# Performance work log

Measured on AMD Instinct MI355X. Metric: run time of the kernel, lower is better.

## Reference

```python
import jax, jax.numpy as jnp
import numpy as np

B, S, D = 1, 2048, 3072
H, DH = 24, 128
ENC, NIP = 512, 64
COND = (512 // 8) * (512 // 8) * 16 // 64  # 1024 cond tokens per lora
RANK, ALPHA, LW, IP_SCALE = 16, 16.0, 1.0, 1.0
EPS = 1e-5


def _rms(x):
    return x * jax.lax.rsqrt(jnp.mean(x * x, axis=-1, keepdims=True) + EPS)


def _to_heads(x):
    b, s, _ = x.shape
    return x.reshape(b, s, H, DH).transpose(0, 2, 1, 3)  # [B,H,S,DH]


def _from_heads(x):
    b, h, s, d = x.shape
    return x.transpose(0, 2, 1, 3).reshape(b, s, h * d)


def _lora(x, dn, up):
    # token mask keeps only the cond block (number=0, n_loras=1 -> last COND tokens)
    y = ((x[:, -COND:, :] @ dn) @ up) * (ALPHA / RANK)
    z = jnp.zeros((x.shape[0], x.shape[1] - COND, up.shape[1]), x.dtype)
    return jnp.concatenate([z, y], axis=1)


def _sdpa(q, k, v, mask=None):
    s = jnp.einsum('bhqd,bhkd->bhqk', q, k) * (1.0 / np.sqrt(DH))
    if mask is not None:
        s = s + mask
    return jnp.einsum('bhqk,bhkd->bhqd', jax.nn.softmax(s, axis=-1), v)


def _forward(hidden_states, encoder_hidden_states, image_emb,
             Wq, bq, Wk, bk, Wv, bv, Waq, baq, Wak, bak, Wav, bav,
             Wo, bo, Wao, bao, Wkip, Wvip,
             lq_dn, lq_up, lk_dn, lk_up, lv_dn, lv_up, lp_dn, lp_up):
    hs, ehs, img = hidden_states, encoder_hidden_states, image_emb
    # context (encoder) projections + RMSNorm on q/k
    eq = _rms(_to_heads(ehs @ Waq + baq))
    ek = _rms(_to_heads(ehs @ Wak + bak))
    ev = _to_heads(ehs @ Wav + bav)
    # main-stream q/k/v with masked LoRA branches
    q = hs @ Wq + bq + LW * _lora(hs, lq_dn, lq_up)
    k = hs @ Wk + bk + LW * _lora(hs, lk_dn, lk_up)
    v = hs @ Wv + bv + LW * _lora(hs, lv_dn, lv_up)
    q = _rms(_to_heads(q))
    k = _rms(_to_heads(k))
    v = _to_heads(v)
    # IP-adapter branch: extra K/V from image_emb, norm_added_k is RMSNorm(128)
    kip = _rms(_to_heads(img @ Wkip))
    vip = _to_heads(img @ Wvip)
    ip_out = _from_heads(_sdpa(q, kip, vip))  # [B,S,D]
    # concat encoder stream ahead of main stream
    q = jnp.concatenate([eq, q], axis=2)
    k = jnp.concatenate([ek, k], axis=2)
    v = jnp.concatenate([ev, v], axis=2)
    SL = ENC + S
    SB = SL - COND  # scaled_block_size
    m = jnp.ones((SL, SL), jnp.float32)
    m = m.at[:SB, :].set(0.0)        # non-cond rows attend everywhere
    m = m.at[SB:, SB:].set(0.0)      # single cond block attends to itself (n_loras=1)
    mask = m * (-1e20)
    out = _from_heads(_sdpa(q, k, v, mask))  # [B,SL,D]
    enc_out = out[:, :ENC, :]
    main = out[:, ENC:, :] + IP_SCALE * ip_out
    main = main @ Wo + bo
    main = main + LW * _lora(main, lp_dn, lp_up)  # proj LoRA (to_out dropout=identity)
    enc_out = enc_out @ Wao + bao
    return jnp.concatenate([enc_out, main], axis=1)  # [B, ENC+S, D]


def setup_inputs():
    key = jax.random.key(0)
    ks = iter(jax.random.split(key, 40))
    w = lambda *sh: jax.random.normal(next(ks), sh, jnp.float32) * 0.02
    return dict(
        hidden_states=jax.random.normal(next(ks), (B, S, D), jnp.float32),
        encoder_hidden_states=jax.random.normal(next(ks), (B, ENC, D), jnp.float32),
        image_emb=jax.random.normal(next(ks), (B, NIP, D), jnp.float32),
        Wq=w(D, D), bq=w(D), Wk=w(D, D), bk=w(D), Wv=w(D, D), bv=w(D),
        Waq=w(D, D), baq=w(D), Wak=w(D, D), bak=w(D), Wav=w(D, D), bav=w(D),
        Wo=w(D, D), bo=w(D), Wao=w(D, D), bao=w(D),
        Wkip=w(D, D), Wvip=w(D, D),
        lq_dn=w(D, RANK), lq_up=w(RANK, D), lk_dn=w(D, RANK), lk_up=w(RANK, D),
        lv_dn=w(D, RANK), lv_up=w(RANK, D), lp_dn=w(D, RANK), lp_up=w(RANK, D),
    )


def reference(hidden_states, encoder_hidden_states, image_emb,
              Wq, bq, Wk, bk, Wv, bv, Waq, baq, Wak, bak, Wav, bav,
              Wo, bo, Wao, bao, Wkip, Wvip,
              lq_dn, lq_up, lk_dn, lk_up, lv_dn, lv_up, lp_dn, lp_up):
    return _forward(hidden_states, encoder_hidden_states, image_emb,
                    Wq, bq, Wk, bk, Wv, bv, Waq, baq, Wak, bak, Wav, bav,
                    Wo, bo, Wao, bao, Wkip, Wvip,
                    lq_dn, lq_up, lk_dn, lk_up, lv_dn, lv_up, lp_dn, lp_up)
```

## Files before the change

### kernel.cpp

```cpp
#include <hip/hip_runtime.h>

typedef unsigned short u16;
typedef short s16x8 __attribute__((ext_vector_type(8)));
typedef float f32x4 __attribute__((ext_vector_type(4)));
typedef const __attribute__((address_space(1))) unsigned int* as1_u32p;
typedef __attribute__((address_space(3))) unsigned int* as3_u32p;

static_assert(sizeof(s16x8) == 16, "");

struct alignas(8) U16x4 { u16 x, y, z, w; };

__device__ __forceinline__ u16 f2bf(float f) {
  union { float f; unsigned u; } c; c.f = f;
  return (u16)((c.u + 0x7fffu + ((c.u >> 16) & 1u)) >> 16);
}
__device__ __forceinline__ float bf2f(u16 h) {
  union { unsigned u; float f; } c; c.u = ((unsigned)h) << 16;
  return c.f;
}
__device__ __forceinline__ void async16(const void* g, void* l) {
  __builtin_amdgcn_global_load_lds((as1_u32p)g, (as3_u32p)l, 16, 0, 0);
}

__launch_bounds__(256)
__global__ void lora_dn3(const float* __restrict__ X, int ldx,
                         const float* __restrict__ d0, const float* __restrict__ d1,
                         const float* __restrict__ d2, float* __restrict__ t) {
  __shared__ float red[4][48];
  const int m = blockIdx.x;
  const float* xr = X + (long)m * ldx;
  float p[48];
#pragma unroll
  for (int r = 0; r < 48; ++r) p[r] = 0.f;
  for (int k = threadIdx.x; k < 3072; k += 256) {
    float a = xr[k];
    const float* e0 = d0 + (long)k * 16;
    const float* e1 = d1 + (long)k * 16;
    const float* e2 = d2 + (long)k * 16;
#pragma unroll
    for (int r = 0; r < 16; ++r) {
      p[r]      += a * e0[r];
      p[16 + r] += a * e1[r];
      p[32 + r] += a * e2[r];
    }
  }
#pragma unroll
  for (int r = 0; r < 48; ++r)
#pragma unroll
    for (int st = 1; st < 64; st <<= 1) p[r] += __shfl_xor(p[r], st, 64);
  int lane = threadIdx.x & 63, w = threadIdx.x >> 6;
  if (lane == 0) {
#pragma unroll
    for (int r = 0; r < 48; ++r) red[w][r] = p[r];
  }
  __syncthreads();
  if (threadIdx.x < 48) {
    int r = threadIdx.x;
    t[(long)m * 48 + r] = red[0][r] + red[1][r] + red[2][r] + red[3][r];
  }
}

__launch_bounds__(256)
__global__ void mega_prep(const float* __restrict__ Waq, const float* __restrict__ Wak,
                          const float* __restrict__ Wav, const float* __restrict__ Wq,
                          const float* __restrict__ Wk, const float* __restrict__ Wv,
                          u16* __restrict__ WTbE, u16* __restrict__ WTbM,
                          const float* __restrict__ Wo, const float* __restrict__ bo,
                          const float* __restrict__ lp_dn, float* __restrict__ Wod,
                          const float* __restrict__ hs, const float* __restrict__ tl,
                          u16* __restrict__ hsb,
                          const float* __restrict__ ehs, u16* __restrict__ ehsb,
                          const float* __restrict__ img, u16* __restrict__ imgb,
                          const float* __restrict__ baq, const float* __restrict__ bak,
                          const float* __restrict__ bav, const float* __restrict__ bq,
                          const float* __restrict__ bk, const float* __restrict__ bv,
                          float* __restrict__ bpk,
                          const float* __restrict__ u0, const float* __restrict__ u1,
                          const float* __restrict__ u2) {
  __shared__ char lmem[4352];
  const int b = blockIdx.x;
  if (b < 55296) {
    int mat = b / 9216, tile = b % 9216;
    const float* src = (mat == 0) ? Waq : (mat == 1) ? Wak : (mat == 2) ? Wav
                       : (mat == 3) ? Wq : (mat == 4) ? Wk : Wv;
    u16* dst = (mat < 3) ? WTbE + (long)mat * 3072 * 3072
                         : WTbM + (long)(mat - 3) * 3072 * 3136;
    const int ldd = (mat < 3) ? 3072 : 3136;
    float (*tile2)[33] = (float(*)[33])lmem;
    int k0 = (tile / 96) * 32, n0 = (tile % 96) * 32;
    int r = threadIdx.x >> 3, c4 = (threadIdx.x & 7) * 4;
    float4 v = *(const float4*)(src + (long)(k0 + r) * 3072 + n0 + c4);
    tile2[r][c4 + 0] = v.x; tile2[r][c4 + 1] = v.y;
    tile2[r][c4 + 2] = v.z; tile2[r][c4 + 3] = v.w;
    __syncthreads();
    U16x4 o{f2bf(tile2[c4 + 0][r]), f2bf(tile2[c4 + 1][r]),
            f2bf(tile2[c4 + 2][r]), f2bf(tile2[c4 + 3][r])};
    *(U16x4*)(dst + (long)(n0 + r) * ldd + k0 + c4) = o;
  } else if (b < 58369) {
    const int m = b - 55296;
    float (*red)[16] = (float(*)[16])lmem;
    const float* xr = (m < 3072) ? Wo + (long)m * 3072 : bo;
    float p[16];
#pragma unroll
    for (int r = 0; r < 16; ++r) p[r] = 0.f;
    for (int k = threadIdx.x; k < 3072; k += 256) {
      float a = xr[k];
      const float* d = lp_dn + (long)k * 16;
#pragma unroll
      for (int r = 0; r < 16; ++r) p[r] += a * d[r];
    }
#pragma unroll
    for (int r = 0; r < 16; ++r)
#pragma unroll
      for (int st = 1; st < 64; st <<= 1) p[r] += __shfl_xor(p[r], st, 64);
    int lane = threadIdx.x & 63, w = threadIdx.x >> 6;
    if (lane == 0) {
#pragma unroll
      for (int r = 0; r < 16; ++r) red[w][r] = p[r];
    }
    __syncthreads();
    if (threadIdx.x < 16) {
      int r = threadIdx.x;
      Wod[(long)m * 16 + r] = red[0][r] + red[1][r] + red[2][r] + red[3][r];
    }
  } else {
    const int pb = b - 58369;
    if (pb < 3136) {
      long idx = (long)pb * 256 + threadIdx.x;
      long m = idx / 392, c = idx % 392;
      U16x4 o0, o1;
      if (c < 384) {
        const float* p = hs + m * 3072 + c * 8;
        float4 a = *(const float4*)p;
        float4 bb = *(const float4*)(p + 4);
        o0 = U16x4{f2bf(a.x), f2bf(a.y), f2bf(a.z), f2bf(a.w)};
        o1 = U16x4{f2bf(bb.x), f2bf(bb.y), f2bf(bb.z), f2bf(bb.w)};
      } else {
        u16 t[8];
#pragma unroll
        for (int i = 0; i < 8; ++i) {
          int r = (int)(c - 384) * 8 + i;
          float v = (m >= 1024 && r < 48) ? tl[(m - 1024) * 48 + r] : 0.f;
          t[i] = f2bf(v);
        }
        o0 = U16x4{t[0], t[1], t[2], t[3]};
        o1 = U16x4{t[4], t[5], t[6], t[7]};
      }
      u16* d = hsb + m * 3136 + c * 8;
      *(U16x4*)d = o0;
      *(U16x4*)(d + 4) = o1;
    } else if (pb < 3904) {
      long i = ((long)(pb - 3136) * 256 + threadIdx.x) * 8;
      float4 a = *(const float4*)(ehs + i);
      float4 bb = *(const float4*)(ehs + i + 4);
      *(U16x4*)(ehsb + i) = U16x4{f2bf(a.x), f2bf(a.y), f2bf(a.z), f2bf(a.w)};
      *(U16x4*)(ehsb + i + 4) = U16x4{f2bf(bb.x), f2bf(bb.y), f2bf(bb.z), f2bf(bb.w)};
    } else if (pb < 4000) {
      long i = ((long)(pb - 3904) * 256 + threadIdx.x) * 8;
      float4 a = *(const float4*)(img + i);
      float4 bb = *(const float4*)(img + i + 4);
      *(U16x4*)(imgb + i) = U16x4{f2bf(a.x), f2bf(a.y), f2bf(a.z), f2bf(a.w)};
      *(U16x4*)(imgb + i + 4) = U16x4{f2bf(bb.x), f2bf(bb.y), f2bf(bb.z), f2bf(bb.w)};
    } else if (pb < 4072) {
      int i = (pb - 4000) * 256 + threadIdx.x;
      if (i < 9216)
        bpk[i] = (i < 3072) ? baq[i] : (i < 6144) ? bak[i - 3072] : bav[i - 6144];
      else {
        int j = i - 9216;
        bpk[i] = (j < 3072) ? bq[j] : (j < 6144) ? bk[j - 3072] : bv[j - 6144];
      }
    } else {
      int idx = (pb - 4072) * 256 + threadIdx.x;
      int n = idx >> 6, i = idx & 63;
      int seg = n / 3072;
      const float* up = (seg == 0) ? u0 : (seg == 1) ? u1 : u2;
      int r = i - seg * 16;
      float v = (r >= 0 && r < 16) ? up[(long)r * 3072 + (n - seg * 3072)] : 0.f;
      WTbM[(long)n * 3136 + 3072 + i] = f2bf(v);
    }
  }
}

struct WT2 { const float* src[2]; u16* dst[2]; };

__launch_bounds__(256)
__global__ void transpose_kv(WT2 args) {
  const float* src = args.src[blockIdx.z];
  u16* dst = args.dst[blockIdx.z];
  __shared__ float tile[32][33];
  int k0 = blockIdx.x * 32, n0 = blockIdx.y * 32;
  int r = threadIdx.x >> 3, c4 = (threadIdx.x & 7) * 4;
  float4 v = *(const float4*)(src + (long)(k0 + r) * 3072 + n0 + c4);
  tile[r][c4 + 0] = v.x; tile[r][c4 + 1] = v.y;
  tile[r][c4 + 2] = v.z; tile[r][c4 + 3] = v.w;
  __syncthreads();
  U16x4 o{f2bf(tile[c4 + 0][r]), f2bf(tile[c4 + 1][r]),
          f2bf(tile[c4 + 2][r]), f2bf(tile[c4 + 3][r])};
  *(U16x4*)(dst + (long)(n0 + r) * 3072 + k0 + c4) = o;
}

__launch_bounds__(256)
__global__ void t_tail(u16* __restrict__ At, const float* __restrict__ Wod) {
  __shared__ float red[4][16];
  const int tok = blockIdx.x;
  u16* tail = At + (long)(512 + tok) * 3136 + 3072;
  if (tok < 1024) {
    if (threadIdx.x < 64) tail[threadIdx.x] = 0;
    return;
  }
  const u16* xr = At + (long)(512 + tok) * 3136;
  float p[16];
#pragma unroll
  for (int r = 0; r < 16; ++r) p[r] = 0.f;
  for (int n = threadIdx.x; n < 3072; n += 256) {
    float a = bf2f(xr[n]);
    const float* wd = Wod + (long)n * 16;
#pragma unroll
    for (int r = 0; r < 16; ++r) p[r] += a * wd[r];
  }
#pragma unroll
  for (int r = 0; r < 16; ++r)
#pragma unroll
    for (int st = 1; st < 64; st <<= 1) p[r] += __shfl_xor(p[r], st, 64);
  int lane = threadIdx.x & 63, w = threadIdx.x >> 6;
  if (lane == 0) {
#pragma unroll
    for (int r = 0; r < 16; ++r) red[w][r] = p[r];
  }
  __syncthreads();
  if (threadIdx.x < 64) {
    if (threadIdx.x < 16) {
      int r = threadIdx.x;
      float t = red[0][r] + red[1][r] + red[2][r] + red[3][r] + Wod[3072L * 16 + r];
      tail[r] = f2bf(t);
    } else {
      tail[threadIdx.x] = 0;
    }
  }
}

template <int BM, int MI, int NI>
__launch_bounds__(256)
__global__ void gemm_f32(const u16* __restrict__ A, int lda,
                         const u16* __restrict__ B, int ldb,
                         float* __restrict__ C, int ldc,
                         const float* __restrict__ bias, int KC, long cstride) {
  constexpr int WCOLS = 128 / (NI * 16);
  constexpr int ABYTES = BM * 128;
  __shared__ char smem[ABYTES + 128 * 128];
  char* As = smem;
  char* Bs = smem + ABYTES;
  const int tid = threadIdx.x;
  const int w = tid >> 6, lane = tid & 63;
  const int lr = lane & 15, lg = lane >> 4;
  const int wr = w / WCOLS, wc = w % WCOLS;
  const int nbx = gridDim.x;
  const int nwg = nbx * gridDim.y;
  const int flat = blockIdx.y * nbx + blockIdx.x;
  const int swz = (flat & 7) * (nwg >> 3) + (flat >> 3);
  const long m0 = (long)(swz % nbx) * BM;
  const long n0 = (long)(swz / nbx) * 128;
  const int k0 = blockIdx.z * KC;
  C += blockIdx.z * cstride;
  f32x4 acc[MI][NI] = {};
  constexpr int ACH = BM / 32;
  for (int kb = k0; kb < k0 + KC; kb += 64) {
    __syncthreads();
#pragma unroll
    for (int i = 0; i < ACH; ++i) {
      int x = (tid + 256 * i) * 16;
      int row = x >> 7;
// ... 202 lines not shown
          int tok = wr * 64 + mi * 16 + lg * 4 + j;
          *(u16*)(smem + tok * 256 + (d2 ^ ((tok & 7) << 4))) =
              f2bf(acc[mi][ni][j] * scl[mi][j]);
        }
      }
  } else {
#pragma unroll
    for (int mi = 0; mi < 4; ++mi)
#pragma unroll
      for (int ni = 0; ni < 4; ++ni) {
        int d = wc * 64 + ni * 16 + lr;
        int tok0b = (wr * 64 + mi * 16 + lg * 4) * 2;
        U16x4 o{f2bf(acc[mi][ni][0]), f2bf(acc[mi][ni][1]),
                f2bf(acc[mi][ni][2]), f2bf(acc[mi][ni][3])};
        *(U16x4*)(smem + d * 256 + (tok0b ^ ((d & 7) << 4))) = o;
      }
  }
  __syncthreads();
#pragma unroll
  for (int i = 0; i < 8; ++i) {
    int x = (tid + 256 * i) * 16;
    int row = x >> 8, col = x & 255;
    s16x8 vdat = *(const s16x8*)(smem + row * 256 + (col ^ ((row & 7) << 4)));
    if (seg < 2) {
      u16* g = (seg == 0 ? Qo : Ko) + ((long)head * 2560 + t0 + m0 + row) * 128;
      *(s16x8*)((char*)g + col) = vdat;
    } else {
      u16* g = VTo + ((long)head * 128 + row) * 2560 + t0 + m0;
      *(s16x8*)((char*)g + col) = vdat;
    }
  }
}

__launch_bounds__(256)
__global__ void gemm_out(const u16* __restrict__ Atok, const u16* __restrict__ Benc,
                         const u16* __restrict__ Bmain, float* __restrict__ outp,
                         const float* __restrict__ bao, const float* __restrict__ bo) {
  __shared__ char smem[128 * 128 + 128 * 128];
  char* As = smem;
  char* Bs = smem + 128 * 128;
  const int tid = threadIdx.x;
  const int w = tid >> 6, lane = tid & 63;
  const int lr = lane & 15, lg = lane >> 4;
  const int wr = w >> 1, wc = w & 1;
  const int flat = blockIdx.y * 20 + blockIdx.x;
  const int swz = (flat & 7) * 60 + (flat >> 3);
  const int mx = swz % 20;
  const long n0 = (long)(swz / 20) * 128;
  const u16* A;
  const u16* B;
  const float* bias;
  float* C;
  int ldb, K;
  long m0;
  if (mx < 4) {
    A = Atok; B = Benc; ldb = 3072; K = 3072; bias = bao; C = outp;
    m0 = (long)mx * 128;
  } else {
    A = Atok + 512L * 3136; B = Bmain; ldb = 3136; K = 3136; bias = bo;
    C = outp + 512L * 3072; m0 = (long)(mx - 4) * 128;
  }
  f32x4 acc[4][4] = {};
  for (int kb = 0; kb < K; kb += 64) {
    __syncthreads();
#pragma unroll
    for (int i = 0; i < 4; ++i) {
// ... 15 lines not shown
#pragma unroll
    for (int kc = 0; kc < 2; ++kc) {
      s16x8 af[4], bfr[4];
#pragma unroll
      for (int mi = 0; mi < 4; ++mi) {
        int row = wr * 64 + mi * 16 + lr;
        int b = ((row << 7) + kc * 64 + lg * 16) ^ ((row & 7) << 4);
        af[mi] = *(const s16x8*)(As + b);
      }
#pragma unroll
      for (int ni = 0; ni < 4; ++ni) {
        int row = wc * 64 + ni * 16 + lr;
        int b = ((row << 7) + kc * 64 + lg * 16) ^ ((row & 7) << 4);
        bfr[ni] = *(const s16x8*)(Bs + b);
      }
#pragma unroll
      for (int mi = 0; mi < 4; ++mi)
#pragma unroll
        for (int ni = 0; ni < 4; ++ni)
          acc[mi][ni] = __builtin_amdgcn_mfma_f32_16x16x32_bf16(af[mi], bfr[ni], acc[mi][ni], 0, 0, 0);
    }
  }
#pragma unroll
  for (int mi = 0; mi < 4; ++mi) {
#pragma unroll
    for (int ni = 0; ni < 4; ++ni) {
      long col = n0 + wc * 64 + ni * 16 + lr;
      float bv = bias[col];
#pragma unroll
      for (int j = 0; j < 4; ++j) {
        long row = m0 + wr * 64 + mi * 16 + lg * 4 + j;
        C[row * 3072 + col] = acc[mi][ni][j] + bv;
      }
    }
  }
}

__launch_bounds__(512, 2)
__global__ void attn_mega(const u16* __restrict__ QB, const u16* __restrict__ KB,
                          const u16* __restrict__ VT, const u16* __restrict__ KipB,
                          const u16* __restrict__ VipT, u16* __restrict__ OutTok,
                          const float* __restrict__ Wao, const float* __restrict__ Wo,
                          u16* __restrict__ WTbE, u16* __restrict__ WTbM,
                          const float* __restrict__ lp_up) {
  __shared__ char smem[81920];
  const int bf = blockIdx.x;
  const int tid = threadIdx.x;
  if (bf >= 480) {
    if (bf < 9696) {
      int t2 = (bf - 480) * 2 + (tid >> 8);
      int mat = t2 / 9216, tile = t2 % 9216;
      const float* src = mat ? Wo : Wao;
      u16* dst = mat ? WTbM : WTbE;
      const int ldd = mat ? 3136 : 3072;
      float (*tl2)[32][33] = (float(*)[32][33])smem;
      int half = tid >> 8, lt = tid & 255;
      int k0 = (tile / 96) * 32, n0t = (tile % 96) * 32;
      int r = lt >> 3, c4 = (lt & 7) * 4;
      float4 v = *(const float4*)(src + (long)(k0 + r) * 3072 + n0t + c4);
      tl2[half][r][c4 + 0] = v.x; tl2[half][r][c4 + 1] = v.y;
      tl2[half][r][c4 + 2] = v.z; tl2[half][r][c4 + 3] = v.w;
      __syncthreads();
      U16x4 o{f2bf(tl2[half][c4 + 0][r]), f2bf(tl2[half][c4 + 1][r]),
              f2bf(tl2[half][c4 + 2][r]), f2bf(tl2[half][c4 + 3][r])};
      *(U16x4*)(dst + (long)(n0t + r) * ldd + k0 + c4) = o;
    } else {
      int idx = (bf - 9696) * 512 + tid;
      int n = idx >> 6, i = idx & 63;
      float v = (i < 16) ? lp_up[(long)i * 3072 + n] : 0.f;
      WTbM[(long)n * 3136 + 3072 + i] = f2bf(v);
    }
    return;
  }
  const int w = tid >> 6, lane = tid & 63;
  const int lr = lane & 15, lg = lane >> 4;
  int h, qb;
  if (bf < 288) { h = bf / 12; qb = bf % 12; }
  else { int s = bf - 288; h = s / 8; qb = 12 + s % 8; }
  const int q0 = qb * 128;
  const bool ip = (q0 >= 512);
  const u16* Qrow = QB + (long)(h * 2560 + q0 + w * 16 + lr) * 128;
  s16x8 qf[4];
#pragma unroll
  for (int dc = 0; dc < 4; ++dc) qf[dc] = *(const s16x8*)(Qrow + dc * 32 + lg * 8);
  f32x4 accO[8] = {};
  float l_r[4] = {0.f, 0.f, 0.f, 0.f};
  const int kv0 = (q0 >= 1536) ? 1536 : 0;
  const float sc = 0.08838834764831845f;

  auto stage_main = [&](int kv, int buf) {
#pragma unroll
    for (int i = 0; i < 2; ++i) {
      int x = (tid + 512 * i) * 16;
      int row = x >> 8;
      int sx = x ^ ((row & 7) << 4);
      async16((const char*)(KB + (long)(h * 2560 + kv + row) * 128) + (sx & 255),
              smem + buf * 16384 + ((i << 13) + (w << 10)));
    }
#pragma unroll
    for (int i = 0; i < 2; ++i) {
      int x = (tid + 512 * i) * 16;
      int row = x >> 7;
      int sx = x ^ ((row & 7) << 4);
      async16((const char*)(VT + (long)(h * 128 + row) * 2560 + kv) + (sx & 127),
              smem + 32768 + buf * 16384 + ((i << 13) + (w << 10)));
    }
  };
  auto stage_ip = [&](int buf) {
#pragma unroll
    for (int i = 0; i < 2; ++i) {
      int x = (tid + 512 * i) * 16;
      int row = x >> 8;
      int sx = x ^ ((row & 7) << 4);
      async16((const char*)(KipB + (long)(h * 64 + row) * 128) + (sx & 255),
              smem + buf * 16384 + ((i << 13) + (w << 10)));
    }
#pragma unroll
    for (int i = 0; i < 2; ++i) {
      int x = (tid + 512 * i) * 16;
      int row = x >> 7;
      int sx = x ^ ((row & 7) << 4);
      async16((const char*)(VipT + (long)(h * 128 + row) * 64) + (sx & 127),
              smem + 32768 + buf * 16384 + ((i << 13) + (w << 10)));
    }
  };

  stage_main(kv0, 0);
  __syncthreads();
  int cur = 0;
  for (int kv = kv0; kv < 2560; kv += 64) {
    if (kv + 64 < 2560) stage_main(kv + 64, cur ^ 1);
    else if (ip) stage_ip(cur ^ 1);
    const char* Ks = smem + cur * 16384;
    const char* Vs = smem + 32768 + cur * 16384;
    char* Pw = smem + 65536 + w * 2048;
    f32x4 s[4] = {};
    __builtin_amdgcn_s_setprio(1);
#pragma unroll
    for (int kt = 0; kt < 4; ++kt)
#pragma unroll
      for (int dc = 0; dc < 4; ++dc) {
        int row = kt * 16 + lr;
        int b = ((row << 8) + dc * 64 + lg * 16) ^ ((row & 7) << 4);
        s16x8 kf = *(const s16x8*)(Ks + b);
        s[kt] = __builtin_amdgcn_mfma_f32_16x16x32_bf16(qf[dc], kf, s[kt], 0, 0, 0);
      }
    __builtin_amdgcn_s_setprio(0);
#pragma unroll
    for (int kt = 0; kt < 4; ++kt)
#pragma unroll
      for (int j = 0; j < 4; ++j) {
        float pv = __expf(fmaf(s[kt][j], sc, -12.0f));
        l_r[j] += pv;
        int prow = lg * 4 + j;
        int b = ((prow << 7) + (kt * 16 + lr) * 2) ^ ((prow & 7) << 4);
        *(u16*)(Pw + b) = f2bf(pv);
      }
    asm volatile("s_waitcnt lgkmcnt(0)" ::: "memory");
    __builtin_amdgcn_s_setprio(1);
#pragma unroll
    for (int kc = 0; kc < 2; ++kc) {
      int pb = ((lr << 7) + kc * 64 + lg * 16) ^ ((lr & 7) << 4);
      s16x8 pf = *(const s16x8*)(Pw + pb);
#pragma unroll
      for (int dt = 0; dt < 8; ++dt) {
        int row = dt * 16 + lr;
        int b = ((row << 7) + kc * 64 + lg * 16) ^ ((row & 7) << 4);
        s16x8 vf = *(const s16x8*)(Vs + b);
        accO[dt] = __builtin_amdgcn_mfma_f32_16x16x32_bf16(pf, vf, accO[dt], 0, 0, 0);
      }
    }
    __builtin_amdgcn_s_setprio(0);
    __syncthreads();
    cur ^= 1;
  }
#pragma unroll
  for (int j = 0; j < 4; ++j) {
#pragma unroll
    for (int st = 1; st < 16; st <<= 1) l_r[j] += __shfl_xor(l_r[j], st, 16);
    l_r[j] = 1.f / l_r[j];
  }
#pragma unroll
  for (int dt = 0; dt < 8; ++dt)
#pragma unroll
    for (int j = 0; j < 4; ++j) accO[dt][j] *= l_r[j];
  if (ip) {
    const char* Ks = smem + cur * 16384;
    const char* Vs = smem + 32768 + cur * 16384;
    char* Pw = smem + 65536 + w * 2048;
    f32x4 s2[4] = {};
#pragma unroll
    for (int kt = 0; kt < 4; ++kt)
#pragma unroll
      for (int dc = 0; dc < 4; ++dc) {
        int row = kt * 16 + lr;
        int b = ((row << 8) + dc * 64 + lg * 16) ^ ((row & 7) << 4);
        s16x8 kf = *(const s16x8*)(Ks + b);
        s2[kt] = __builtin_amdgcn_mfma_f32_16x16x32_bf16(qf[dc], kf, s2[kt], 0, 0, 0);
      }
    float p2[4][4];
    float l2[4] = {0.f, 0.f, 0.f, 0.f};
#pragma unroll
    for (int kt = 0; kt < 4; ++kt)
#pragma unroll
      for (int j = 0; j < 4; ++j) {
        float pv = __expf(fmaf(s2[kt][j], sc, -12.0f));
        p2[kt][j] = pv;
        l2[j] += pv;
      }
#pragma unroll
    for (int j = 0; j < 4; ++j) {
#pragma unroll
      for (int st = 1; st < 16; st <<= 1) l2[j] += __shfl_xor(l2[j], st, 16);
      l2[j] = 1.f / l2[j];
    }
#pragma unroll
    for (int kt = 0; kt < 4; ++kt)
#pragma unroll
      for (int j = 0; j < 4; ++j) {
        int prow = lg * 4 + j;
        int b = ((prow << 7) + (kt * 16 + lr) * 2) ^ ((prow & 7) << 4);
        *(u16*)(Pw + b) = f2bf(p2[kt][j] * l2[j]);
      }
    asm volatile("s_waitcnt lgkmcnt(0)" ::: "memory");
#pragma unroll
    for (int kc = 0; kc < 2; ++kc) {
      int pb = ((lr << 7) + kc * 64 + lg * 16) ^ ((lr & 7) << 4);
      s16x8 pf = *(const s16x8*)(Pw + pb);
#pragma unroll
      for (int dt = 0; dt < 8; ++dt) {
        int row = dt * 16 + lr;
        int b = ((row << 7) + kc * 64 + lg * 16) ^ ((row & 7) << 4);
        s16x8 vf = *(const s16x8*)(Vs + b);
        accO[dt] = __builtin_amdgcn_mfma_f32_16x16x32_bf16(pf, vf, accO[dt], 0, 0, 0);
      }
    }
  }
#pragma unroll
  for (int j = 0; j < 4; ++j) {
    long tok = q0 + w * 16 + lg * 4 + j;
#pragma unroll
    for (int dt = 0; dt < 8; ++dt) {
      long col = h * 128 + dt * 16 + lr;
      OutTok[tok * 3136 + col] = f2bf(accO[dt][j]);
    }
  }
}


extern "C" void kernel_launch(void* const* d_in, const int* in_sizes, int n_in,
                              void* d_out, int out_size, void* d_ws, size_t ws_size,
                              hipStream_t stream) {
  const float* hs    = (const float*)d_in[0];
  const float* ehs   = (const float*)d_in[1];
  const float* img   = (const float*)d_in[2];
  const float* Wq    = (const float*)d_in[3];
  const float* bq    = (const float*)d_in[4];
  const float* Wk    = (const float*)d_in[5];
  const float* bk    = (const float*)d_in[6];
  const float* Wv    = (const float*)d_in[7];
  const float* bv    = (const float*)d_in[8];
  const float* Waq   = (const float*)d_in[9];
  const float* baq   = (const float*)d_in[10];
  const float* Wak   = (const float*)d_in[11];
  const float* bak   = (const float*)d_in[12];
  const float* Wav   = (const float*)d_in[13];
  const float* bav   = (const float*)d_in[14];
  const float* Wo    = (const float*)d_in[15];
  const float* bo    = (const float*)d_in[16];
  const float* Wao   = (const float*)d_in[17];
  const float* bao   = (const float*)d_in[18];
  const float* Wkip  = (const float*)d_in[19];
  const float* Wvip  = (const float*)d_in[20];
  const float* lq_dn = (const float*)d_in[21];
  const float* lq_up = (const float*)d_in[22];
  const float* lk_dn = (const float*)d_in[23];
  const float* lk_up = (const float*)d_in[24];
  const float* lv_dn = (const float*)d_in[25];
  const float* lv_up = (const float*)d_in[26];
  const float* lp_dn = (const float*)d_in[27];
  const float* lp_up = (const float*)d_in[28];
  float* outp = (float*)d_out;

  char* ws = (char*)d_ws;
  size_t off = 0;
  auto take = [&](size_t b) { char* p = ws + off; off += (b + 255) & ~(size_t)255; return p; };
  u16*   WTbE = (u16*)take(3LL * 3072 * 3072 * 2);
  u16*   WTbM = (u16*)take(3LL * 3072 * 3136 * 2);
  u16*   hsb  = (u16*)take(2048LL * 3136 * 2);
  u16*   ehsb = (u16*)take(512LL * 3072 * 2);
  u16*   imgb = (u16*)take(64LL * 3072 * 2);
  u16*   VTf  = (u16*)take(24LL * 128 * 2560 * 2);
  float* IP0  = (float*)take(4LL * 64 * 6144 * 4);
  u16*   KipB = (u16*)take(24LL * 64 * 128 * 2);
  u16*   VipB = (u16*)take(24LL * 64 * 128 * 2);
  u16*   VipT = (u16*)take(24LL * 128 * 64 * 2);
  float* bpk  = (float*)take(2 * 9216 * 4);
  float* tl   = (float*)take(1024LL * 48 * 4);
  float* Wod  = (float*)take(3073LL * 16 * 4);
  u16* QBf = (u16*)d_out;
  u16* KBf = (u16*)d_out + 24LL * 2560 * 128;
  u16* AttnTok = hsb;
  u16* E1 = WTbE + 3072LL * 3072;
  u16* E2 = WTbE + 2 * 3072LL * 3072;

  lora_dn3<<<1024, 256, 0, stream>>>(hs + 1024LL * 3072, 3072, lq_dn, lk_dn, lv_dn, tl);
  mega_prep<<<64745, 256, 0, stream>>>(Waq, Wak, Wav, Wq, Wk, Wv, WTbE, WTbM,
                                       Wo, bo, lp_dn, Wod,
                                       hs, tl, hsb, ehs, ehsb, img, imgb,
                                       baq, bak, bav, bq, bk, bv, bpk,
                                       lq_up, lk_up, lv_up);

  gemm_qkv<<<dim3(20, 72), 256, 0, stream>>>(ehsb, hsb, WTbE, WTbM, QBf, KBf, VTf, bpk);

  {
    WT2 a;
    a.src[0] = Wkip; a.dst[0] = E1;
    a.src[1] = Wvip; a.dst[1] = E2;
    transpose_kv<<<dim3(96, 96, 2), 256, 0, stream>>>(a);
  }
  gemm_f32<64, 4, 2><<<dim3(1, 48, 4), 256, 0, stream>>>(imgb, 3072, E1, 3072, IP0, 6144,
                                                          nullptr, 768, 64LL * 6144);
  rms_ip<<<128, 256, 0, stream>>>(IP0, KipB, VipB);
  transpose_v<<<dim3(2, 4, 24), 256, 0, stream>>>(VipB, VipT, 64);

  attn_mega<<<10080, 512, 0, stream>>>(QBf, KBf, VTf, KipB, VipT, AttnTok,
                                       Wao, Wo, WTbE, WTbM, lp_up);

  t_tail<<<2048, 256, 0, stream>>>(AttnTok, Wod);
  gemm_out<<<dim3(20, 24), 256, 0, stream>>>(AttnTok, WTbE, WTbM, outp, bao, bo);
}
```

Baseline: 577.2 us.

## Rebalance kernel fusion: fold LoRA-down into prep, split attention from weight transposes

Moves the LoRA down-projection into the mega_prep launch and adds a small t_hs kernel that writes its results into the hsb tail columns. The Wo/Wao transposes and lp_up packing move out of the attention mega-kernel into a new ttail_mega launch that also runs the tail projection, so attention now launches only its 480 compute blocks. Transpose_kv becomes a flat 1D grid. The aim is to stop the attention kernel from also carrying thousands of transpose blocks and to cut one launch, in exchange for an extra small kernel and different overlap between the transpose work and attention.

```diff
diff --git a/kernel.cpp b/kernel.cpp
--- a/kernel.cpp
+++ b/kernel.cpp
@@ -20,44 +20,6 @@
 }
 __device__ __forceinline__ void async16(const void* g, void* l) {
   __builtin_amdgcn_global_load_lds((as1_u32p)g, (as3_u32p)l, 16, 0, 0);
-}
-
-__launch_bounds__(256)
-__global__ void lora_dn3(const float* __restrict__ X, int ldx,
-                         const float* __restrict__ d0, const float* __restrict__ d1,
-                         const float* __restrict__ d2, float* __restrict__ t) {
-  __shared__ float red[4][48];
-  const int m = blockIdx.x;
-  const float* xr = X + (long)m * ldx;
-  float p[48];
-#pragma unroll
-  for (int r = 0; r < 48; ++r) p[r] = 0.f;
-  for (int k = threadIdx.x; k < 3072; k += 256) {
-    float a = xr[k];
-    const float* e0 = d0 + (long)k * 16;
-    const float* e1 = d1 + (long)k * 16;
-    const float* e2 = d2 + (long)k * 16;
-#pragma unroll
-    for (int r = 0; r < 16; ++r) {
-      p[r]      += a * e0[r];
-      p[16 + r] += a * e1[r];
-      p[32 + r] += a * e2[r];
-    }
-  }
-#pragma unroll
-  for (int r = 0; r < 48; ++r)
-#pragma unroll
-    for (int st = 1; st < 64; st <<= 1) p[r] += __shfl_xor(p[r], st, 64);
-  int lane = threadIdx.x & 63, w = threadIdx.x >> 6;
-  if (lane == 0) {
-#pragma unroll
-    for (int r = 0; r < 48; ++r) red[w][r] = p[r];
-  }
-  __syncthreads();
-  if (threadIdx.x < 48) {
-    int r = threadIdx.x;
-    t[(long)m * 48 + r] = red[0][r] + red[1][r] + red[2][r] + red[3][r];
-  }
 }
 
 __launch_bounds__(256)
@@ -67,8 +29,9 @@
                           u16* __restrict__ WTbE, u16* __restrict__ WTbM,
                           const float* __restrict__ Wo, const float* __restrict__ bo,
                           const float* __restrict__ lp_dn, float* __restrict__ Wod,
-                          const float* __restrict__ hs, const float* __restrict__ tl,
-                          u16* __restrict__ hsb,
+                          const float* __restrict__ d0, const float* __restrict__ d1,
+                          const float* __restrict__ d2, float* __restrict__ tl,
+                          const float* __restrict__ hs, u16* __restrict__ hsb,
                           const float* __restrict__ ehs, u16* __restrict__ ehsb,
                           const float* __restrict__ img, u16* __restrict__ imgb,
                           const float* __restrict__ baq, const float* __restrict__ bak,
@@ -96,8 +59,41 @@
     U16x4 o{f2bf(tile2[c4 + 0][r]), f2bf(tile2[c4 + 1][r]),
             f2bf(tile2[c4 + 2][r]), f2bf(tile2[c4 + 3][r])};
     *(U16x4*)(dst + (long)(n0 + r) * ldd + k0 + c4) = o;
-  } else if (b < 58369) {
+  } else if (b < 56320) {
     const int m = b - 55296;
+    float (*red)[48] = (float(*)[48])lmem;
+    const float* xr = hs + (long)(1024 + m) * 3072;
+    float p[48];
+#pragma unroll
+    for (int r = 0; r < 48; ++r) p[r] = 0.f;
+    for (int k = threadIdx.x; k < 3072; k += 256) {
+      float a = xr[k];
+      const float* e0 = d0 + (long)k * 16;
+      const float* e1 = d1 + (long)k * 16;
+      const float* e2 = d2 + (long)k * 16;
+#pragma unroll
+      for (int r = 0; r < 16; ++r) {
+        p[r]      += a * e0[r];
+        p[16 + r] += a * e1[r];
+        p[32 + r] += a * e2[r];
+      }
+    }
+#pragma unroll
+    for (int r = 0; r < 48; ++r)
+#pragma unroll
+      for (int st = 1; st < 64; st <<= 1) p[r] += __shfl_xor(p[r], st, 64);
+    int lane = threadIdx.x & 63, w = threadIdx.x >> 6;
+    if (lane == 0) {
+#pragma unroll
+      for (int r = 0; r < 48; ++r) red[w][r] = p[r];
+    }
+    __syncthreads();
+    if (threadIdx.x < 48) {
+      int r = threadIdx.x;
+      tl[(long)m * 48 + r] = red[0][r] + red[1][r] + red[2][r] + red[3][r];
+    }
+  } else if (b < 59393) {
+    const int m = b - 56320;
     float (*red)[16] = (float(*)[16])lmem;
     const float* xr = (m < 3072) ? Wo + (long)m * 3072 : bo;
     float p[16];
@@ -124,27 +120,17 @@
       Wod[(long)m * 16 + r] = red[0][r] + red[1][r] + red[2][r] + red[3][r];
     }
   } else {
-    const int pb = b - 58369;
+    const int pb = b - 59393;
     if (pb < 3136) {
       long idx = (long)pb * 256 + threadIdx.x;
       long m = idx / 392, c = idx % 392;
-      U16x4 o0, o1;
+      U16x4 o0{0, 0, 0, 0}, o1{0, 0, 0, 0};
       if (c < 384) {
         const float* p = hs + m * 3072 + c * 8;
         float4 a = *(const float4*)p;
         float4 bb = *(const float4*)(p + 4);
         o0 = U16x4{f2bf(a.x), f2bf(a.y), f2bf(a.z), f2bf(a.w)};
         o1 = U16x4{f2bf(bb.x), f2bf(bb.y), f2bf(bb.z), f2bf(bb.w)};
-      } else {
-        u16 t[8];
-#pragma unroll
-        for (int i = 0; i < 8; ++i) {
-          int r = (int)(c - 384) * 8 + i;
-          float v = (m >= 1024 && r < 48) ? tl[(m - 1024) * 48 + r] : 0.f;
-          t[i] = f2bf(v);
-        }
-        o0 = U16x4{t[0], t[1], t[2], t[3]};
-        o1 = U16x4{t[4], t[5], t[6], t[7]};
       }
       u16* d = hsb + m * 3136 + c * 8;
       *(U16x4*)d = o0;
@@ -181,14 +167,22 @@
   }
 }
 
-struct WT2 { const float* src[2]; u16* dst[2]; };
-
 __launch_bounds__(256)
-__global__ void transpose_kv(WT2 args) {
-  const float* src = args.src[blockIdx.z];
-  u16* dst = args.dst[blockIdx.z];
+__global__ void t_hs(const float* __restrict__ tl, u16* __restrict__ hsb) {
+  int idx = blockIdx.x * 256 + threadIdx.x;
+  int m = idx / 48, r = idx % 48;
+  hsb[(long)(1024 + m) * 3136 + 3072 + r] = f2bf(tl[m * 48 + r]);
+}
+
+__launch_bounds__(256)
+__global__ void transpose2(const float* __restrict__ Wkip, const float* __restrict__ Wvip,
+                           u16* __restrict__ E1) {
   __shared__ float tile[32][33];
-  int k0 = blockIdx.x * 32, n0 = blockIdx.y * 32;
+  const int b = blockIdx.x;
+  int mat = b / 9216, t = b % 9216;
+  const float* src = mat ? Wvip : Wkip;
+  u16* dst = E1 + (long)mat * 3072 * 3072;
+  int k0 = (t / 96) * 32, n0 = (t % 96) * 32;
   int r = threadIdx.x >> 3, c4 = (threadIdx.x & 7) * 4;
   float4 v = *(const float4*)(src + (long)(k0 + r) * 3072 + n0 + c4);
   tile[r][c4 + 0] = v.x; tile[r][c4 + 1] = v.y;
@@ -197,46 +191,6 @@
   U16x4 o{f2bf(tile[c4 + 0][r]), f2bf(tile[c4 + 1][r]),
           f2bf(tile[c4 + 2][r]), f2bf(tile[c4 + 3][r])};
   *(U16x4*)(dst + (long)(n0 + r) * 3072 + k0 + c4) = o;
-}
-
-__launch_bounds__(256)
-__global__ void t_tail(u16* __restrict__ At, const float* __restrict__ Wod) {
-  __shared__ float red[4][16];
-  const int tok = blockIdx.x;
-  u16* tail = At + (long)(512 + tok) * 3136 + 3072;
-  if (tok < 1024) {
-    if (threadIdx.x < 64) tail[threadIdx.x] = 0;
-    return;
-  }
-  const u16* xr = At + (long)(512 + tok) * 3136;
-  float p[16];
-#pragma unroll
-  for (int r = 0; r < 16; ++r) p[r] = 0.f;
-  for (int n = threadIdx.x; n < 3072; n += 256) {
-    float a = bf2f(xr[n]);
-    const float* wd = Wod + (long)n * 16;
-#pragma unroll
-    for (int r = 0; r < 16; ++r) p[r] += a * wd[r];
-  }
-#pragma unroll
-  for (int r = 0; r < 16; ++r)
-#pragma unroll
-    for (int st = 1; st < 64; st <<= 1) p[r] += __shfl_xor(p[r], st, 64);
-  int lane = threadIdx.x & 63, w = threadIdx.x >> 6;
-  if (lane == 0) {
-#pragma unroll
-    for (int r = 0; r < 16; ++r) red[w][r] = p[r];
-  }
-  __syncthreads();
-  if (threadIdx.x < 64) {
-    if (threadIdx.x < 16) {
-      int r = threadIdx.x;
-      float t = red[0][r] + red[1][r] + red[2][r] + red[3][r] + Wod[3072L * 16 + r];
-      tail[r] = f2bf(t);
-    } else {
-      tail[threadIdx.x] = 0;
-    }
-  }
 }
 
 template <int BM, int MI, int NI>
@@ -505,6 +459,255 @@
   }
 }
 
+__launch_bounds__(512, 2)
+__global__ void attn_fused(const u16* __restrict__ QB, const u16* __restrict__ KB,
+                           const u16* __restrict__ VT, const u16* __restrict__ KipB,
+                           const u16* __restrict__ VipT, u16* __restrict__ OutTok) {
+  __shared__ char smem[81920];
+  const int bf = blockIdx.x;
+  const int tid = threadIdx.x;
+  const int w = tid >> 6, lane = tid & 63;
+  const int lr = lane & 15, lg = lane >> 4;
+  int h, qb;
+  if (bf < 288) { h = bf / 12; qb = bf % 12; }
+  else { int s = bf - 288; h = s / 8; qb = 12 + s % 8; }
+  const int q0 = qb * 128;
+  const bool ip = (q0 >= 512);
+  const u16* Qrow = QB + (long)(h * 2560 + q0 + w * 16 + lr) * 128;
+  s16x8 qf[4];
+#pragma unroll
+  for (int dc = 0; dc < 4; ++dc) qf[dc] = *(const s16x8*)(Qrow + dc * 32 + lg * 8);
+  f32x4 accO[8] = {};
+  float l_r[4] = {0.f, 0.f, 0.f, 0.f};
+  const int kv0 = (q0 >= 1536) ? 1536 : 0;
+  const float sc = 0.08838834764831845f;
+
+  auto stage_main = [&](int kv, int buf) {
+#pragma unroll
+    for (int i = 0; i < 2; ++i) {
+      int x = (tid + 512 * i) * 16;
+      int row = x >> 8;
+      int sx = x ^ ((row & 7) << 4);
+      async16((const char*)(KB + (long)(h * 2560 + kv + row) * 128) + (sx & 255),
+              smem + buf * 16384 + ((i << 13) + (w << 10)));
+    }
+#pragma unroll
+    for (int i = 0; i < 2; ++i) {
+      int x = (tid + 512 * i) * 16;
+      int row = x >> 7;
+      int sx = x ^ ((row & 7) << 4);
+      async16((const char*)(VT + (long)(h * 128 + row) * 2560 + kv) + (sx & 127),
+              smem + 32768 + buf * 16384 + ((i << 13) + (w << 10)));
+    }
+  };
+  auto stage_ip = [&](int buf) {
+#pragma unroll
+    for (int i = 0; i < 2; ++i) {
+      int x = (tid + 512 * i) * 16;
+      int row = x >> 8;
+      int sx = x ^ ((row & 7) << 4);
+      async16((const char*)(KipB + (long)(h * 64 + row) * 128) + (sx & 255),
+              smem + buf * 16384 + ((i << 13) + (w << 10)));
+    }
+#pragma unroll
+    for (int i = 0; i < 2; ++i) {
+      int x = (tid + 512 * i) * 16;
+      int row = x >> 7;
+      int sx = x ^ ((row & 7) << 4);
+      async16((const char*)(VipT + (long)(h * 128 + row) * 64) + (sx & 127),
+              smem + 32768 + buf * 16384 + ((i << 13) + (w << 10)));
+    }
+  };
+
+  stage_main(kv0, 0);
+  __syncthreads();
+  int cur = 0;
+  for (int kv = kv0; kv < 2560; kv += 64) {
+    if (kv + 64 < 2560) stage_main(kv + 64, cur ^ 1);
+    else if (ip) stage_ip(cur ^ 1);
+    const char* Ks = smem + cur * 16384;
+    const char* Vs = smem + 32768 + cur * 16384;
+    char* Pw = smem + 65536 + w * 2048;
+    f32x4 s[4] = {};
+    __builtin_amdgcn_s_setprio(1);
+#pragma unroll
+    for (int kt = 0; kt < 4; ++kt)
+#pragma unroll
+      for (int dc = 0; dc < 4; ++dc) {
+        int row = kt * 16 + lr;
+        int b = ((row << 8) + dc * 64 + lg * 16) ^ ((row & 7) << 4);
+        s16x8 kf = *(const s16x8*)(Ks + b);
+        s[kt] = __builtin_amdgcn_mfma_f32_16x16x32_bf16(qf[dc], kf, s[kt], 0, 0, 0);
+      }
+    __builtin_amdgcn_s_setprio(0);
+#pragma unroll
+    for (int kt = 0; kt < 4; ++kt)
+#pragma unroll
+      for (int j = 0; j < 4; ++j) {
+        float pv = __expf(fmaf(s[kt][j], sc, -12.0f));
+        l_r[j] += pv;
+        int prow = lg * 4 + j;
+        int b = ((prow << 7) + (kt * 16 + lr) * 2) ^ ((prow & 7) << 4);
+        *(u16*)(Pw + b) = f2bf(pv);
+      }
+    asm volatile("s_waitcnt lgkmcnt(0)" ::: "memory");
+    __builtin_amdgcn_s_setprio(1);
+#pragma unroll
+    for (int kc = 0; kc < 2; ++kc) {
+      int pb = ((lr << 7) + kc * 64 + lg * 16) ^ ((lr & 7) << 4);
+      s16x8 pf = *(const s16x8*)(Pw + pb);
+#pragma unroll
+      for (int dt = 0; dt < 8; ++dt) {
+        int row = dt * 16 + lr;
+        int b = ((row << 7) + kc * 64 + lg * 16) ^ ((row & 7) << 4);
+        s16x8 vf = *(const s16x8*)(Vs + b);
+        accO[dt] = __builtin_amdgcn_mfma_f32_16x16x32_bf16(pf, vf, accO[dt], 0, 0, 0);
+      }
+    }
+    __builtin_amdgcn_s_setprio(0);
+    __syncthreads();
+    cur ^= 1;
+  }
+#pragma unroll
+  for (int j = 0; j < 4; ++j) {
+#pragma unroll
+    for (int st = 1; st < 16; st <<= 1) l_r[j] += __shfl_xor(l_r[j], st, 16);
+    l_r[j] = 1.f / l_r[j];
+  }
+#pragma unroll
+  for (int dt = 0; dt < 8; ++dt)
+#pragma unroll
+    for (int j = 0; j < 4; ++j) accO[dt][j] *= l_r[j];
+  if (ip) {
+    const char* Ks = smem + cur * 16384;
+    const char* Vs = smem + 32768 + cur * 16384;
+    char* Pw = smem + 65536 + w * 2048;
+    f32x4 s2[4] = {};
+#pragma unroll
+    for (int kt = 0; kt < 4; ++kt)
+#pragma unroll
+      for (int dc = 0; dc < 4; ++dc) {
+        int row = kt * 16 + lr;
+        int b = ((row << 8) + dc * 64 + lg * 16) ^ ((row & 7) << 4);
+        s16x8 kf = *(const s16x8*)(Ks + b);
+        s2[kt] = __builtin_amdgcn_mfma_f32_16x16x32_bf16(qf[dc], kf, s2[kt], 0, 0, 0);
+      }
+    float p2[4][4];
+    float l2[4] = {0.f, 0.f, 0.f, 0.f};
+#pragma unroll
+    for (int kt = 0; kt < 4; ++kt)
+#pragma unroll
+      for (int j = 0; j < 4; ++j) {
+        float pv = __expf(fmaf(s2[kt][j], sc, -12.0f));
+        p2[kt][j] = pv;
+        l2[j] += pv;
+      }
+#pragma unroll
+    for (int j = 0; j < 4; ++j) {
+#pragma unroll
+      for (int st = 1; st < 16; st <<= 1) l2[j] += __shfl_xor(l2[j], st, 16);
+      l2[j] = 1.f / l2[j];
+    }
+#pragma unroll
+    for (int kt = 0; kt < 4; ++kt)
+#pragma unroll
+      for (int j = 0; j < 4; ++j) {
+        int prow = lg * 4 + j;
+        int b = ((prow << 7) + (kt * 16 + lr) * 2) ^ ((prow & 7) << 4);
+        *(u16*)(Pw + b) = f2bf(p2[kt][j] * l2[j]);
+      }
+    asm volatile("s_waitcnt lgkmcnt(0)" ::: "memory");
+#pragma unroll
+    for (int kc = 0; kc < 2; ++kc) {
+      int pb = ((lr << 7) + kc * 64 + lg * 16) ^ ((lr & 7) << 4);
+      s16x8 pf = *(const s16x8*)(Pw + pb);
+#pragma unroll
+      for (int dt = 0; dt < 8; ++dt) {
+        int row = dt * 16 + lr;
+        int b = ((row << 7) + kc * 64 + lg * 16) ^ ((row & 7) << 4);
+        s16x8 vf = *(const s16x8*)(Vs + b);
+        accO[dt] = __builtin_amdgcn_mfma_f32_16x16x32_bf16(pf, vf, accO[dt], 0, 0, 0);
+      }
+    }
+  }
+#pragma unroll
+  for (int j = 0; j < 4; ++j) {
+    long tok = q0 + w * 16 + lg * 4 + j;
+#pragma unroll
+    for (int dt = 0; dt < 8; ++dt) {
+      long col = h * 128 + dt * 16 + lr;
+      OutTok[tok * 3136 + col] = f2bf(accO[dt][j]);
+    }
+  }
+}
+
+__launch_bounds__(256)
+__global__ void ttail_mega(u16* __restrict__ At, const float* __restrict__ Wod,
+                           const float* __restrict__ Wao, const float* __restrict__ Wo,
+                           u16* __restrict__ WTbE, u16* __restrict__ WTbM,
+                           const float* __restrict__ lp_up) {
+  __shared__ char lmem[4352];
+  const int b = blockIdx.x;
+  if (b < 18432) {
+    int mat = b / 9216, tile = b % 9216;
+    const float* src = mat ? Wo : Wao;
+    u16* dst = mat ? WTbM : WTbE;
+    const int ldd = mat ? 3136 : 3072;
+    float (*tile2)[33] = (float(*)[33])lmem;
+    int k0 = (tile / 96) * 32, n0 = (tile % 96) * 32;
+    int r = threadIdx.x >> 3, c4 = (threadIdx.x & 7) * 4;
+    float4 v = *(const float4*)(src + (long)(k0 + r) * 3072 + n0 + c4);
+    tile2[r][c4 + 0] = v.x; tile2[r][c4 + 1] = v.y;
+    tile2[r][c4 + 2] = v.z; tile2[r][c4 + 3] = v.w;
+    __syncthreads();
+    U16x4 o{f2bf(tile2[c4 + 0][r]), f2bf(tile2[c4 + 1][r]),
+            f2bf(tile2[c4 + 2][r]), f2bf(tile2[c4 + 3][r])};
+    *(U16x4*)(dst + (long)(n0 + r) * ldd + k0 + c4) = o;
+  } else if (b < 19200) {
+    int idx = (b - 18432) * 256 + threadIdx.x;
+    int n = idx >> 6, i = idx & 63;
+    float v = (i < 16) ? lp_up[(long)i * 3072 + n] : 0.f;
+    WTbM[(long)n * 3136 + 3072 + i] = f2bf(v);
+  } else {
+    float (*red)[16] = (float(*)[16])lmem;
+    const int tok = b - 19200;
+    u16* tail = At + (long)(512 + tok) * 3136 + 3072;
+    if (tok < 1024) {
+      if (threadIdx.x < 64) tail[threadIdx.x] = 0;
+      return;
+    }
+    const u16* xr = At + (long)(512 + tok) * 3136;
+    float p[16];
+#pragma unroll
+    for (int r = 0; r < 16; ++r) p[r] = 0.f;
+    for (int n = threadIdx.x; n < 3072; n += 256) {
+      float a = bf2f(xr[n]);
+      const float* wd = Wod + (long)n * 16;
+#pragma unroll
+      for (int r = 0; r < 16; ++r) p[r] += a * wd[r];
+    }
+#pragma unroll
+    for (int r = 0; r < 16; ++r)
+#pragma unroll
+      for (int st = 1; st < 64; st <<= 1) p[r] += __shfl_xor(p[r], st, 64);
+    int lane = threadIdx.x & 63, w = threadIdx.x >> 6;
+    if (lane == 0) {
+#pragma unroll
+      for (int r = 0; r < 16; ++r) red[w][r] = p[r];
+    }
+    __syncthreads();
+    if (threadIdx.x < 64) {
+      if (threadIdx.x < 16) {
+        int r = threadIdx.x;
+        float t = red[0][r] + red[1][r] + red[2][r] + red[3][r] + Wod[3072L * 16 + r];
+        tail[r] = f2bf(t);
+      } else {
+        tail[threadIdx.x] = 0;
+      }
+    }
+  }
+}
+
 __launch_bounds__(256)
 __global__ void gemm_out(const u16* __restrict__ Atok, const u16* __restrict__ Benc,
                          const u16* __restrict__ Bmain, float* __restrict__ outp,
@@ -586,217 +789,6 @@
         long row = m0 + wr * 64 + mi * 16 + lg * 4 + j;
         C[row * 3072 + col] = acc[mi][ni][j] + bv;
       }
-    }
-  }
-}
-
-__launch_bounds__(512, 2)
-__global__ void attn_mega(const u16* __restrict__ QB, const u16* __restrict__ KB,
-                          const u16* __restrict__ VT, const u16* __restrict__ KipB,
-                          const u16* __restrict__ VipT, u16* __restrict__ OutTok,
-                          const float* __restrict__ Wao, const float* __restrict__ Wo,
-                          u16* __restrict__ WTbE, u16* __restrict__ WTbM,
-                          const float* __restrict__ lp_up) {
-  __shared__ char smem[81920];
-  const int bf = blockIdx.x;
-  const int tid = threadIdx.x;
-  if (bf >= 480) {
-    if (bf < 9696) {
-      int t2 = (bf - 480) * 2 + (tid >> 8);
-      int mat = t2 / 9216, tile = t2 % 9216;
-      const float* src = mat ? Wo : Wao;
-      u16* dst = mat ? WTbM : WTbE;
-      const int ldd = mat ? 3136 : 3072;
-      float (*tl2)[32][33] = (float(*)[32][33])smem;
-      int half = tid >> 8, lt = tid & 255;
-      int k0 = (tile / 96) * 32, n0t = (tile % 96) * 32;
-      int r = lt >> 3, c4 = (lt & 7) * 4;
-      float4 v = *(const float4*)(src + (long)(k0 + r) * 3072 + n0t + c4);
-      tl2[half][r][c4 + 0] = v.x; tl2[half][r][c4 + 1] = v.y;
-      tl2[half][r][c4 + 2] = v.z; tl2[half][r][c4 + 3] = v.w;
-      __syncthreads();
-      U16x4 o{f2bf(tl2[half][c4 + 0][r]), f2bf(tl2[half][c4 + 1][r]),
-              f2bf(tl2[half][c4 + 2][r]), f2bf(tl2[half][c4 + 3][r])};
-      *(U16x4*)(dst + (long)(n0t + r) * ldd + k0 + c4) = o;
-    } else {
-      int idx = (bf - 9696) * 512 + tid;
-      int n = idx >> 6, i = idx & 63;
-      float v = (i < 16) ? lp_up[(long)i * 3072 + n] : 0.f;
-      WTbM[(long)n * 3136 + 3072 + i] = f2bf(v);
-    }
-    return;
-  }
-  const int w = tid >> 6, lane = tid & 63;
-  const int lr = lane & 15, lg = lane >> 4;
-  int h, qb;
-  if (bf < 288) { h = bf / 12; qb = bf % 12; }
-  else { int s = bf - 288; h = s / 8; qb = 12 + s % 8; }
-  const int q0 = qb * 128;
-  const bool ip = (q0 >= 512);
-  const u16* Qrow = QB + (long)(h * 2560 + q0 + w * 16 + lr) * 128;
-  s16x8 qf[4];
-#pragma unroll
-  for (int dc = 0; dc < 4; ++dc) qf[dc] = *(const s16x8*)(Qrow + dc * 32 + lg * 8);
-  f32x4 accO[8] = {};
-  float l_r[4] = {0.f, 0.f, 0.f, 0.f};
-  const int kv0 = (q0 >= 1536) ? 1536 : 0;
-  const float sc = 0.08838834764831845f;
-
-  auto stage_main = [&](int kv, int buf) {
-#pragma unroll
-    for (int i = 0; i < 2; ++i) {
-      int x = (tid + 512 * i) * 16;
-      int row = x >> 8;
-      int sx = x ^ ((row & 7) << 4);
-      async16((const char*)(KB + (long)(h * 2560 + kv + row) * 128) + (sx & 255),
-              smem + buf * 16384 + ((i << 13) + (w << 10)));
-    }
-#pragma unroll
-    for (int i = 0; i < 2; ++i) {
-      int x = (tid + 512 * i) * 16;
-      int row = x >> 7;
-      int sx = x ^ ((row & 7) << 4);
-      async16((const char*)(VT + (long)(h * 128 + row) * 2560 + kv) + (sx & 127),
-              smem + 32768 + buf * 16384 + ((i << 13) + (w << 10)));
-    }
-  };
-  auto stage_ip = [&](int buf) {
-#pragma unroll
-    for (int i = 0; i < 2; ++i) {
-      int x = (tid + 512 * i) * 16;
-      int row = x >> 8;
-      int sx = x ^ ((row & 7) << 4);
-      async16((const char*)(KipB + (long)(h * 64 + row) * 128) + (sx & 255),
-              smem + buf * 16384 + ((i << 13) + (w << 10)));
-    }
-#pragma unroll
-    for (int i = 0; i < 2; ++i) {
-      int x = (tid + 512 * i) * 16;
-      int row = x >> 7;
-      int sx = x ^ ((row & 7) << 4);
-      async16((const char*)(VipT + (long)(h * 128 + row) * 64) + (sx & 127),
-              smem + 32768 + buf * 16384 + ((i << 13) + (w << 10)));
-    }
-  };
-
-  stage_main(kv0, 0);
-  __syncthreads();
-  int cur = 0;
-  for (int kv = kv0; kv < 2560; kv += 64) {
-    if (kv + 64 < 2560) stage_main(kv + 64, cur ^ 1);
-    else if (ip) stage_ip(cur ^ 1);
-    const char* Ks = smem + cur * 16384;
-    const char* Vs = smem + 32768 + cur * 16384;
-    char* Pw = smem + 65536 + w * 2048;
-    f32x4 s[4] = {};
-    __builtin_amdgcn_s_setprio(1);
-#pragma unroll
-    for (int kt = 0; kt < 4; ++kt)
-#pragma unroll
-      for (int dc = 0; dc < 4; ++dc) {
-        int row = kt * 16 + lr;
-        int b = ((row << 8) + dc * 64 + lg * 16) ^ ((row & 7) << 4);
-        s16x8 kf = *(const s16x8*)(Ks + b);
-        s[kt] = __builtin_amdgcn_mfma_f32_16x16x32_bf16(qf[dc], kf, s[kt], 0, 0, 0);
-      }
-    __builtin_amdgcn_s_setprio(0);
-#pragma unroll
-    for (int kt = 0; kt < 4; ++kt)
-#pragma unroll
-      for (int j = 0; j < 4; ++j) {
-        float pv = __expf(fmaf(s[kt][j], sc, -12.0f));
-        l_r[j] += pv;
-        int prow = lg * 4 + j;
-        int b = ((prow << 7) + (kt * 16 + lr) * 2) ^ ((prow & 7) << 4);
-        *(u16*)(Pw + b) = f2bf(pv);
-      }
-    asm volatile("s_waitcnt lgkmcnt(0)" ::: "memory");
-    __builtin_amdgcn_s_setprio(1);
-#pragma unroll
-    for (int kc = 0; kc < 2; ++kc) {
-      int pb = ((lr << 7) + kc * 64 + lg * 16) ^ ((lr & 7) << 4);
-      s16x8 pf = *(const s16x8*)(Pw + pb);
-#pragma unroll
-      for (int dt = 0; dt < 8; ++dt) {
-        int row = dt * 16 + lr;
-        int b = ((row << 7) + kc * 64 + lg * 16) ^ ((row & 7) << 4);
-        s16x8 vf = *(const s16x8*)(Vs + b);
-        accO[dt] = __builtin_amdgcn_mfma_f32_16x16x32_bf16(pf, vf, accO[dt], 0, 0, 0);
-      }
-    }
-    __builtin_amdgcn_s_setprio(0);
-    __syncthreads();
-    cur ^= 1;
-  }
-#pragma unroll
-  for (int j = 0; j < 4; ++j) {
-#pragma unroll
-    for (int st = 1; st < 16; st <<= 1) l_r[j] += __shfl_xor(l_r[j], st, 16);
-    l_r[j] = 1.f / l_r[j];
-  }
-#pragma unroll
-  for (int dt = 0; dt < 8; ++dt)
-#pragma unroll
-    for (int j = 0; j < 4; ++j) accO[dt][j] *= l_r[j];
-  if (ip) {
-    const char* Ks = smem + cur * 16384;
-    const char* Vs = smem + 32768 + cur * 16384;
-    char* Pw = smem + 65536 + w * 2048;
-    f32x4 s2[4] = {};
-#pragma unroll
-    for (int kt = 0; kt < 4; ++kt)
-#pragma unroll
-      for (int dc = 0; dc < 4; ++dc) {
-        int row = kt * 16 + lr;
-        int b = ((row << 8) + dc * 64 + lg * 16) ^ ((row & 7) << 4);
-        s16x8 kf = *(const s16x8*)(Ks + b);
-        s2[kt] = __builtin_amdgcn_mfma_f32_16x16x32_bf16(qf[dc], kf, s2[kt], 0, 0, 0);
-      }
-    float p2[4][4];
-    float l2[4] = {0.f, 0.f, 0.f, 0.f};
-#pragma unroll
-    for (int kt = 0; kt < 4; ++kt)
-#pragma unroll
-      for (int j = 0; j < 4; ++j) {
-        float pv = __expf(fmaf(s2[kt][j], sc, -12.0f));
-        p2[kt][j] = pv;
-        l2[j] += pv;
-      }
-#pragma unroll
-    for (int j = 0; j < 4; ++j) {
-#pragma unroll
-      for (int st = 1; st < 16; st <<= 1) l2[j] += __shfl_xor(l2[j], st, 16);
-      l2[j] = 1.f / l2[j];
-    }
-#pragma unroll
-    for (int kt = 0; kt < 4; ++kt)
-#pragma unroll
-      for (int j = 0; j < 4; ++j) {
-        int prow = lg * 4 + j;
-        int b = ((prow << 7) + (kt * 16 + lr) * 2) ^ ((prow & 7) << 4);
-        *(u16*)(Pw + b) = f2bf(p2[kt][j] * l2[j]);
-      }
-    asm volatile("s_waitcnt lgkmcnt(0)" ::: "memory");
-#pragma unroll
-    for (int kc = 0; kc < 2; ++kc) {
-      int pb = ((lr << 7) + kc * 64 + lg * 16) ^ ((lr & 7) << 4);
-      s16x8 pf = *(const s16x8*)(Pw + pb);
-#pragma unroll
-      for (int dt = 0; dt < 8; ++dt) {
-        int row = dt * 16 + lr;
-        int b = ((row << 7) + kc * 64 + lg * 16) ^ ((row & 7) << 4);
-        s16x8 vf = *(const s16x8*)(Vs + b);
-        accO[dt] = __builtin_amdgcn_mfma_f32_16x16x32_bf16(pf, vf, accO[dt], 0, 0, 0);
-      }
-    }
-  }
-#pragma unroll
-  for (int j = 0; j < 4; ++j) {
-    long tok = q0 + w * 16 + lg * 4 + j;
-#pragma unroll
-    for (int dt = 0; dt < 8; ++dt) {
-      long col = h * 128 + dt * 16 + lr;
-      OutTok[tok * 3136 + col] = f2bf(accO[dt][j]);
     }
   }
 }
@@ -856,31 +848,27 @@
   u16* KBf = (u16*)d_out + 24LL * 2560 * 128;
   u16* AttnTok = hsb;
   u16* E1 = WTbE + 3072LL * 3072;
-  u16* E2 = WTbE + 2 * 3072LL * 3072;
-
-  lora_dn3<<<1024, 256, 0, stream>>>(hs + 1024LL * 3072, 3072, lq_dn, lk_dn, lv_dn, tl);
-  mega_prep<<<64745, 256, 0, stream>>>(Waq, Wak, Wav, Wq, Wk, Wv, WTbE, WTbM,
+
+  mega_prep<<<65769, 256, 0, stream>>>(Waq, Wak, Wav, Wq, Wk, Wv, WTbE, WTbM,
                                        Wo, bo, lp_dn, Wod,
-                                       hs, tl, hsb, ehs, ehsb, img, imgb,
+                                       lq_dn, lk_dn, lv_dn, tl,
+                                       hs, hsb, ehs, ehsb, img, imgb,
                                        baq, bak, bav, bq, bk, bv, bpk,
                                        lq_up, lk_up, lv_up);
+  t_hs<<<192, 256, 0, stream>>>(tl, hsb);
 
   gemm_qkv<<<dim3(20, 72), 256, 0, stream>>>(ehsb, hsb, WTbE, WTbM, QBf, KBf, VTf, bpk);
 
-  {
-    WT2 a;
-    a.src[0] = Wkip; a.dst[0] = E1;
-    a.src[1] = Wvip; a.dst[1] = E2;
-    transpose_kv<<<dim3(96, 96, 2), 256, 0, stream>>>(a);
-  }
+  transpose2<<<18432, 256, 0, stream>>>(Wkip, Wvip, E1);
+
   gemm_f32<64, 4, 2><<<dim3(1, 48, 4), 256, 0, stream>>>(imgb, 3072, E1, 3072, IP0, 6144,
                                                           nullptr, 768, 64LL * 6144);
   rms_ip<<<128, 256, 0, stream>>>(IP0, KipB, VipB);
   transpose_v<<<dim3(2, 4, 24), 256, 0, stream>>>(VipB, VipT, 64);
 
-  attn_mega<<<10080, 512, 0, stream>>>(QBf, KBf, VTf, KipB, VipT, AttnTok,
-                                       Wao, Wo, WTbE, WTbM, lp_up);
-
-  t_tail<<<2048, 256, 0, stream>>>(AttnTok, Wod);
+  attn_fused<<<480, 512, 0, stream>>>(QBf, KBf, VTf, KipB, VipT, AttnTok);
+
+  ttail_mega<<<21248, 256, 0, stream>>>(AttnTok, Wod, Wao, Wo, WTbE, WTbM, lp_up);
+
   gemm_out<<<dim3(20, 24), 256, 0, stream>>>(AttnTok, WTbE, WTbM, outp, bao, bo);
 }
```

After: 599.8 us. 3.9% more time.
